# Performance work log

Measured on AMD Instinct MI355X. Metric: run time of the kernel, lower is better.

## Reference

```python
import jax, jax.numpy as jnp
import numpy as np

SIZE = 128
RATIO = 0.5

def setup_inputs() -> dict:
    key = jax.random.key(0)
    k1, k2, k3 = jax.random.split(key, 3)
    B, D, K = 16, 256, 18
    assp_features = jax.random.normal(k1, (B, D, SIZE, SIZE), dtype=jnp.float32)
    prototypes = jax.random.normal(k2, (B, K, D), dtype=jnp.float32)
    n_samp = int(SIZE * SIZE * RATIO)
    # sample without replacement, matching np.random.choice(replace=False)
    random_indices = jax.random.permutation(k3, SIZE * SIZE)[:n_samp].astype(jnp.int64)
    return {"assp_features": assp_features, "prototypes": prototypes,
            "random_indices": random_indices}

def reference(assp_features, prototypes, random_indices):
    # assp_features: [B, D, H, W], prototypes: [B, K, D], random_indices: [N]
    size = assp_features.shape[-1]
    x = random_indices // size  # [N]
    y = random_indices % size   # [N]
    f = assp_features[:, :, x, y]            # [B, D, N] gathered pixel features
    # squared L2 distances [B, N, K]; argmin of ||p-f||_2 == argmin of squared dist
    p2 = jnp.sum(prototypes * prototypes, axis=-1)       # [B, K]
    f2 = jnp.sum(f * f, axis=1)                          # [B, N]
    cross = jnp.einsum('bdn,bkd->bnk', f, prototypes)    # [B, N, K]
    d2 = p2[:, None, :] - 2.0 * cross + f2[:, :, None]
    idx = jnp.argmin(d2, axis=-1)                        # [B, N]
    nearest = jnp.take_along_axis(prototypes, idx[..., None], axis=1)  # [B, N, D]
    out = assp_features.at[:, :, x, y].set(jnp.swapaxes(nearest, 1, 2))
    return out
```

## Files before the change

### kernel.cpp

```cpp
#include <hip/hip_runtime.h>

constexpr int B = 16;
constexpr int D = 256;
constexpr int K = 18;
constexpr int KH = 9;
constexpr int SZ = 128;
constexpr int S = SZ * SZ;
constexpr int N = S / 2;
constexpr int PB = 512;

__global__ __launch_bounds__(256) void prep2_kernel(
    const float* __restrict__ proto,
    const int* __restrict__ idx,
    unsigned char* __restrict__ mask,
    double* __restrict__ p2) {
  const int blk = blockIdx.x;
  if (blk < 32) {
    mask[idx[blk * 256 + threadIdx.x]] = 1;
  } else {
    const int row  = (blk - 32) * 4 + (threadIdx.x >> 6);
    const int lane = threadIdx.x & 63;
    const float4 v = *(const float4*)(proto + (size_t)row * D + lane * 4);
    double s = (double)v.x * (double)v.x + (double)v.y * (double)v.y
             + (double)v.z * (double)v.z + (double)v.w * (double)v.w;
#pragma unroll
    for (int off = 1; off < 64; off <<= 1)
      s += __shfl_xor(s, off, 64);
    if (lane == 0) p2[row] = s;
  }
}

__global__ __launch_bounds__(256, 2) void fused_kernel(
    const float* __restrict__ assp,
    const float* __restrict__ proto,
    const double* __restrict__ p2,
    const unsigned char* __restrict__ mask,
    float* __restrict__ out) {
  __shared__ double spd[D][K];
  __shared__ float  spf[D][K];
  __shared__ unsigned char skst[PB];

  const int b     = blockIdx.x & 15;
  const int chunk = blockIdx.x >> 4;
  const int bpos0 = chunk * PB;
  const int tid   = threadIdx.x;

  const float* pbr = proto + (size_t)b * K * D;
  for (int i = tid; i < K * D; i += 256) {
    const int k = i >> 8, d = i & 255;
    const float v = pbr[i];
    spd[d][k] = (double)v;
    spf[d][k] = v;
  }
  __syncthreads();

  const int lane = tid & 63;
  const int wv   = tid >> 6;
  const int kh   = lane & 1;
  const int pair = lane >> 1;
  const int lpos = wv * 128 + pair * 4;
  const float* fin = assp + (size_t)b * D * S + bpos0 + lpos;

  double acc[4][KH];
#pragma unroll
  for (int jp = 0; jp < 4; ++jp)
#pragma unroll
    for (int j = 0; j < KH; ++j) acc[jp][j] = 0.0;

  for (int d0 = 0; d0 < D; d0 += 8) {
    float4 fv[8];
#pragma unroll
    for (int jd = 0; jd < 8; ++jd)
      fv[jd] = *(const float4*)(fin + (size_t)(d0 + jd) * S);
#pragma unroll
    for (int jd = 0; jd < 8; ++jd) {
      const double f0 = (double)fv[jd].x;
      const double f1 = (double)fv[jd].y;
      const double f2 = (double)fv[jd].z;
      const double f3 = (double)fv[jd].w;
      const double* pr = &spd[d0 + jd][kh * KH];
#pragma unroll
      for (int j = 0; j < KH; ++j) {
        const double pk = pr[j];
        acc[0][j] += f0 * pk;
        acc[1][j] += f1 * pk;
        acc[2][j] += f2 * pk;
        acc[3][j] += f3 * pk;
      }
    }
  }

  const double* p2h = p2 + (size_t)b * K + kh * KH;
  int kst[4];
#pragma unroll
  for (int jp = 0; jp < 4; ++jp) {
    double bb = 1e300;
    int bj = 0;
#pragma unroll
    for (int j = 0; j < KH; ++j) {
      const double d2 = p2h[j] - 2.0 * acc[jp][j];
      if (d2 < bb) { bb = d2; bj = j; }
    }
    const int myk = kh * KH + bj;
    const double ob = __shfl_xor(bb, 1, 64);
    const int    ok = __shfl_xor(myk, 1, 64);
    const double bLow  = kh ? ob  : bb;
    const int    kLow  = kh ? ok  : myk;
    const double bHigh = kh ? bb  : ob;
    const int    kHigh = kh ? myk : ok;
    kst[jp] = (bLow <= bHigh) ? kLow : kHigh;
  }

  if (kh == 0) {
    uchar4 kk;
    kk.x = (unsigned char)kst[0];
    kk.y = (unsigned char)kst[1];
    kk.z = (unsigned char)kst[2];
    kk.w = (unsigned char)kst[3];
    *(uchar4*)&skst[lpos] = kk;
  }
  __syncthreads();

  const int p = 2 * tid;
  const uchar2 kk2 = *(const uchar2*)&skst[p];
  const uchar2 m   = *(const uchar2*)(mask + bpos0 + p);
  const float* fin2 = assp + (size_t)b * D * S + bpos0 + p;
  float*       op   = out  + (size_t)b * D * S + bpos0 + p;
  const int k0 = kk2.x, k1 = kk2.y;

  for (int d0 = D - 8; d0 >= 0; d0 -= 8) {
    float2 fa[8];
#pragma unroll
    for (int jd = 0; jd < 8; ++jd)
      fa[jd] = *(const float2*)(fin2 + (size_t)(d0 + jd) * S);
#pragma unroll
    for (int jd = 0; jd < 8; ++jd) {
      const int d = d0 + jd;
      float2 o;
      o.x = m.x ? spf[d][k0] : fa[jd].x;
      o.y = m.y ? spf[d][k1] : fa[jd].y;
      *(float2*)(op + (size_t)d * S) = o;
    }
  }
}

extern "C" void kernel_launch(void* const* d_in, const int* in_sizes, int n_in,
                              void* d_out, int out_size, void* d_ws, size_t ws_size,
                              hipStream_t stream) {
  const float* assp  = (const float*)d_in[0];
  const float* proto = (const float*)d_in[1];
  const int*   idx   = (const int*)d_in[2];
  float* out = (float*)d_out;

  unsigned char* mask = (unsigned char*)d_ws;
  double*        p2   = (double*)((char*)d_ws + S);

  hipMemsetAsync(mask, 0, S, stream);
  prep2_kernel<<<104, 256, 0, stream>>>(proto, idx, mask, p2);
  fused_kernel<<<B * (S / PB), 256, 0, stream>>>(assp, proto, p2, mask, out);
}
```

Before: 201.2 us.

## Double-buffer feature loads and rotate channel start per block in distance loop

The distance-accumulation loop now double-buffers its global loads, fetching the next group of eight channels into a second register set while the current group is computed. Each block also starts at a rotated channel offset derived from its chunk and batch index, which spreads concurrent blocks across different DRAM regions. This is meant to hide load latency and reduce memory channel conflicts. It doubles the feature registers, which may cut occupancy. The rotated summation order can change the fp64 accumulation slightly.

```diff
diff --git a/kernel.cpp b/kernel.cpp
--- a/kernel.cpp
+++ b/kernel.cpp
@@ -29,6 +29,26 @@
     if (lane == 0) p2[row] = s;
   }
 }
+
+#define COMPUTE_GROUP(FV, DBASE)                                   \
+  {                                                                \
+    _Pragma("unroll")                                              \
+    for (int jd = 0; jd < 8; ++jd) {                               \
+      const double f0 = (double)FV[jd].x;                          \
+      const double f1 = (double)FV[jd].y;                          \
+      const double f2 = (double)FV[jd].z;                          \
+      const double f3 = (double)FV[jd].w;                          \
+      const double* pr = &spd[(DBASE) + jd][kh * KH];              \
+      _Pragma("unroll")                                            \
+      for (int j = 0; j < KH; ++j) {                               \
+        const double pk = pr[j];                                   \
+        acc[0][j] += f0 * pk;                                      \
+        acc[1][j] += f1 * pk;                                      \
+        acc[2][j] += f2 * pk;                                      \
+        acc[3][j] += f3 * pk;                                      \
+      }                                                            \
+    }                                                              \
+  }
 
 __global__ __launch_bounds__(256, 2) void fused_kernel(
     const float* __restrict__ assp,
@@ -67,27 +87,28 @@
 #pragma unroll
     for (int j = 0; j < KH; ++j) acc[jp][j] = 0.0;
 
-  for (int d0 = 0; d0 < D; d0 += 8) {
-    float4 fv[8];
+  const int rot = (chunk + 4 * b) & 31;
+  float4 fvA[8], fvB[8];
+
+  int dA = rot * 8;
+#pragma unroll
+  for (int jd = 0; jd < 8; ++jd)
+    fvA[jd] = *(const float4*)(fin + (size_t)(dA + jd) * S);
+
+  for (int tt = 0; tt < 32; tt += 2) {
+    const int dB = ((tt + 1 + rot) & 31) * 8;
 #pragma unroll
     for (int jd = 0; jd < 8; ++jd)
-      fv[jd] = *(const float4*)(fin + (size_t)(d0 + jd) * S);
+      fvB[jd] = *(const float4*)(fin + (size_t)(dB + jd) * S);
+    COMPUTE_GROUP(fvA, dA);
+    const int dA2 = ((tt + 2 + rot) & 31) * 8;
+    if (tt + 2 < 32) {
 #pragma unroll
-    for (int jd = 0; jd < 8; ++jd) {
-      const double f0 = (double)fv[jd].x;
-      const double f1 = (double)fv[jd].y;
-      const double f2 = (double)fv[jd].z;
-      const double f3 = (double)fv[jd].w;
-      const double* pr = &spd[d0 + jd][kh * KH];
-#pragma unroll
-      for (int j = 0; j < KH; ++j) {
-        const double pk = pr[j];
-        acc[0][j] += f0 * pk;
-        acc[1][j] += f1 * pk;
-        acc[2][j] += f2 * pk;
-        acc[3][j] += f3 * pk;
-      }
+      for (int jd = 0; jd < 8; ++jd)
+        fvA[jd] = *(const float4*)(fin + (size_t)(dA2 + jd) * S);
     }
+    COMPUTE_GROUP(fvB, dB);
+    dA = dA2;
   }
 
   const double* p2h = p2 + (size_t)b * K + kh * KH;
```

Measured after the change: 481.6 us. +139.3%, slower.
